# Performance work log

Hardware: AMD Instinct MI355X
Metric: run time of the kernel (lower is better)

Reference implementation:

```python
import jax, jax.numpy as jnp
import numpy as np

B, S, D_IN, D_OUT, BLK = 2, 2048, 4096, 16384, 32
NBLK = D_IN // BLK  # 128


def setup_inputs() -> dict:
    key = jax.random.key(0)
    k_x, k_q, k_s, k_b = jax.random.split(key, 4)
    x = jax.random.normal(k_x, (B, S, D_IN), dtype=jnp.float32)
    # GGML Q8_0: signed 8-bit quants per block of 32
    qs = jax.random.randint(k_q, (D_OUT, NBLK, BLK), -128, 128, dtype=jnp.int32)
    # per-block scales (stand-in for the fp16 'd' field); small magnitude
    scales = jax.random.uniform(k_s, (D_OUT, NBLK), dtype=jnp.float32) * 0.02
    bias = jax.random.normal(k_b, (D_OUT,), dtype=jnp.float32)
    return {"x": x, "qs": qs, "scales": scales, "bias": bias}


def reference(x, qs, scales, bias):
    # _materialize_weight: block dequantize (d * q per block) then cast to input dtype
    # qs: [O, NBLK, BLK], scales: [O, NBLK] -> W: [O, D_IN]
    W = (scales[:, :, None] * qs.astype(x.dtype)).reshape(D_OUT, D_IN)
    # host Linear: y = x @ W^T + b
    y = jnp.einsum('bsd,od->bso', x, W) + bias
    return y
```

## Files before the change

kernel.cpp:

```cpp
#include <hip/hip_runtime.h>
#include <cstdint>
#include <cstddef>

#define M_DIM 4096
#define N_DIM 16384
#define K_DIM 4096
#define NBLK_Q 128

#define BM 256
#define BN 256
#define BK 32
#define KSTEPS (K_DIM / BK)
#define BUFB 16384
#define NBUF 4

typedef int i32x4 __attribute__((ext_vector_type(4)));
typedef int i32x16 __attribute__((ext_vector_type(16)));

#define SFENCE() __builtin_amdgcn_sched_barrier(0)
#define BAR() __builtin_amdgcn_s_barrier()
#define WAITVM(n) asm volatile("s_waitcnt vmcnt(" #n ")")
#define WAITLG0() asm volatile("s_waitcnt lgkmcnt(0)")

__global__ __launch_bounds__(256) void quant_x(const float* __restrict__ x,
                                               char* __restrict__ A8S,
                                               float* __restrict__ sxr) {
  const int m = blockIdx.x;
  const int t = threadIdx.x;
  const float* xr = x + (size_t)m * K_DIM + t * 16;
  float4 v[4];
#pragma unroll
  for (int i = 0; i < 4; ++i) v[i] = ((const float4*)xr)[i];
  float amax = 0.f;
#pragma unroll
  for (int i = 0; i < 4; ++i)
    amax = fmaxf(amax, fmaxf(fmaxf(fabsf(v[i].x), fabsf(v[i].y)),
                             fmaxf(fabsf(v[i].z), fabsf(v[i].w))));
#pragma unroll
  for (int off = 32; off; off >>= 1) amax = fmaxf(amax, __shfl_xor(amax, off, 64));
  __shared__ float wmax[4];
  if ((t & 63) == 0) wmax[t >> 6] = amax;
  __syncthreads();
  amax = fmaxf(fmaxf(wmax[0], wmax[1]), fmaxf(wmax[2], wmax[3]));
  const float inv = 127.0f / amax;
  if (t == 0) sxr[m] = amax / 127.0f;
  unsigned d[4];
#pragma unroll
  for (int i = 0; i < 4; ++i) {
    int q0 = (int)rintf(v[i].x * inv), q1 = (int)rintf(v[i].y * inv);
    int q2 = (int)rintf(v[i].z * inv), q3 = (int)rintf(v[i].w * inv);
    d[i] = (q0 & 0xff) | ((q1 & 0xff) << 8) | ((q2 & 0xff) << 16) | ((q3 & 0xff) << 24);
  }
  const int k32 = t >> 1, kg = t & 1;
  const int mtile = m >> 8, mm = m & 255, m32 = mm >> 5, r = mm & 31;
  int4* dst = (int4*)(A8S + ((size_t)(mtile * 128 + k32)) * 8192 + m32 * 1024 + kg * 512 + r * 16);
  *dst = make_int4(d[0], d[1], d[2], d[3]);
}

__global__ __launch_bounds__(256) void pack_w8(const int* __restrict__ qs,
                                               const float* __restrict__ scales,
                                               char* __restrict__ B8S,
                                               float* __restrict__ swc) {
  const int o = blockIdx.x * 4 + (threadIdx.x >> 6);
  const int l = threadIdx.x & 63;
  const float s0 = scales[(size_t)o * NBLK_Q + l];
  const float s1 = scales[(size_t)o * NBLK_Q + 64 + l];
  float S = fmaxf(s0, s1);
#pragma unroll
  for (int off = 32; off; off >>= 1) S = fmaxf(S, __shfl_xor(S, off, 64));
  if (l == 0) swc[o] = S;
  const float rS = 1.0f / S;
  const int nt = o >> 8, col = o & 255, n32 = col >> 5, c = col & 31;
#pragma unroll
  for (int h = 0; h < 2; ++h) {
    const int nb = l + 64 * h;
    const float ratio = ((h == 0) ? s0 : s1) * rS;
    const int4* q = (const int4*)(qs + ((size_t)o * NBLK_Q + nb) * 32);
    unsigned d[8];
#pragma unroll
    for (int g = 0; g < 8; ++g) {
      int4 v = q[g];
      int a0 = (int)rintf((float)v.x * ratio);
      int a1 = (int)rintf((float)v.y * ratio);
      int a2 = (int)rintf((float)v.z * ratio);
      int a3 = (int)rintf((float)v.w * ratio);
      d[g] = (a0 & 0xff) | ((a1 & 0xff) << 8) | ((a2 & 0xff) << 16) | ((a3 & 0xff) << 24);
    }
    char* dst = B8S + ((size_t)(nt * 128 + nb)) * 8192 + n32 * 1024 + c * 16;
    ((int4*)dst)[0] = make_int4(d[0], d[1], d[2], d[3]);
    ((int4*)(dst + 512))[0] = make_int4(d[4], d[5], d[6], d[7]);
  }
}

__global__ __launch_bounds__(512, 2) void gemm_i8(
    const char* __restrict__ A8S, const char* __restrict__ B8S,
    const float* __restrict__ sxr, const float* __restrict__ swc,
    const float* __restrict__ bias, float* __restrict__ C) {
  __shared__ __align__(16) char lds[NBUF * BUFB];

  const int tid = threadIdx.x;
  const int w = tid >> 6;
  const int l = tid & 63;
  const int wm = w >> 2;
  const int wn = w & 3;

  const int bid = blockIdx.x;
  const int xcd = bid & 7;
  const int k = bid >> 3;
  const int mtile = xcd * 2 + (k & 1);
  const int ntile = k >> 1;
  const int brow = mtile * BM;
  const int bcol = ntile * BN;

  const char* srcA = A8S + (size_t)mtile * 128 * 8192 + w * 1024 + l * 16;
  const char* srcB = B8S + (size_t)ntile * 128 * 8192 + w * 1024 + l * 16;
  const int doffA = w * 1024 + l * 16;
  const int doffB = 8192 + w * 1024 + l * 16;
  const int roffA = wm * 4096 + l * 16;
  const int roffB = 8192 + wn * 2048 + l * 16;

  i32x16 acc[4][2] = {};
  i32x4 a0[4], b0[2], a1[4], b1[2];
  int4 gA0, gB0, gA1, gB1;

  {
    int4 ta0 = *(const int4*)(srcA);
    int4 tb0 = *(const int4*)(srcB);
    int4 ta1 = *(const int4*)(srcA + 8192);
    int4 tb1 = *(const int4*)(srcB + 8192);
    *(int4*)(lds + doffA) = ta0;
    *(int4*)(lds + doffB) = tb0;
    *(int4*)(lds + BUFB + doffA) = ta1;
    *(int4*)(lds + BUFB + doffB) = tb1;
    gA0 = *(const int4*)(srcA + 2 * 8192);
    gB0 = *(const int4*)(srcB + 2 * 8192);
    WAITLG0();
    SFENCE(); BAR(); SFENCE();
#pragma unroll
    for (int i = 0; i < 4; ++i)
      a0[i] = *(const i32x4*)(lds + roffA + i * 1024);
#pragma unroll
    for (int j = 0; j < 2; ++j)
      b0[j] = *(const i32x4*)(lds + roffB + j * 1024);
  }

#define STEP(KT, CA, CB, NA, NB, WA, WB, LA, LB)                               \
  do {                                                                         \
    const char* rb = lds + (((KT) + 1) & 3) * BUFB;                            \
    NA[0] = *(const i32x4*)(rb + roffA);                                       \
    NA[1] = *(const i32x4*)(rb + roffA + 1024);                                \
    NA[2] = *(const i32x4*)(rb + roffA + 2048);                                \
    NA[3] = *(const i32x4*)(rb + roffA + 3072);                                \
    NB[0] = *(const i32x4*)(rb + roffB);                                       \
    NB[1] = *(const i32x4*)(rb + roffB + 1024);                                \
    {                                                                          \
      const int ql = ((KT) + 3 > KSTEPS - 1) ? (KSTEPS - 1) : ((KT) + 3);      \
      LA = *(const int4*)(srcA + (size_t)ql * 8192);                           \
      LB = *(const int4*)(srcB + (size_t)ql * 8192);                           \
    }                                                                          \
    SFENCE();                                                                  \
    __builtin_amdgcn_s_setprio(1);                                             \
    acc[0][0] = __builtin_amdgcn_mfma_i32_32x32x32_i8(CA[0], CB[0], acc[0][0], 0, 0, 0); \
    acc[0][1] = __builtin_amdgcn_mfma_i32_32x32x32_i8(CA[0], CB[1], acc[0][1], 0, 0, 0); \
    acc[1][0] = __builtin_amdgcn_mfma_i32_32x32x32_i8(CA[1], CB[0], acc[1][0], 0, 0, 0); \
    acc[1][1] = __builtin_amdgcn_mfma_i32_32x32x32_i8(CA[1], CB[1], acc[1][1], 0, 0, 0); \
    acc[2][0] = __builtin_amdgcn_mfma_i32_32x32x32_i8(CA[2], CB[0], acc[2][0], 0, 0, 0); \
    acc[2][1] = __builtin_amdgcn_mfma_i32_32x32x32_i8(CA[2], CB[1], acc[2][1], 0, 0, 0); \
    acc[3][0] = __builtin_amdgcn_mfma_i32_32x32x32_i8(CA[3], CB[0], acc[3][0], 0, 0, 0); \
    acc[3][1] = __builtin_amdgcn_mfma_i32_32x32x32_i8(CA[3], CB[1], acc[3][1], 0, 0, 0); \
    __builtin_amdgcn_s_setprio(0);                                             \
    SFENCE();                                                                  \
    WAITVM(2);                                                                 \
    {                                                                          \
      char* wb = lds + (((KT) + 2) & 3) * BUFB;                                \
      *(int4*)(wb + doffA) = WA;                                               \
      *(int4*)(wb + doffB) = WB;                                               \
    }                                                                          \
    SFENCE();                                                                  \
    WAITLG0();                                                                 \
    SFENCE(); BAR(); SFENCE();                                                 \
  } while (0)

  for (int kt = 0; kt < KSTEPS; kt += 2) {
    STEP(kt, a0, b0, a1, b1, gA0, gB0, gA1, gB1);
    STEP(kt + 1, a1, b1, a0, b0, gA1, gB1, gA0, gB0);
  }
#undef STEP

#pragma unroll
  for (int i = 0; i < 4; ++i) {
    const int rb = brow + wm * 128 + i * 32 + 4 * (l >> 5);
#pragma unroll
    for (int j = 0; j < 2; ++j) {
      const int col = bcol + wn * 64 + j * 32 + (l & 31);
      const float Sw = swc[col];
      const float bv = bias[col];
#pragma unroll
      for (int r = 0; r < 16; ++r) {
        const int row = rb + (r & 3) + 8 * (r >> 2);
        C[(size_t)row * N_DIM + col] = (float)acc[i][j][r] * (sxr[row] * Sw) + bv;
      }
    }
  }
}

__global__ void naive_gemm(const float* __restrict__ x, const int* __restrict__ qs,
                           const float* __restrict__ scales, const float* __restrict__ bias,
                           float* __restrict__ y) {
  size_t idx = (size_t)blockIdx.x * 256 + threadIdx.x;
  if (idx >= (size_t)M_DIM * N_DIM) return;
  int o = (int)(idx % N_DIM);
  size_t m = idx / N_DIM;
  const float* xr = x + m * K_DIM;
  const int* q = qs + (size_t)o * K_DIM;
  const float* sc = scales + (size_t)o * NBLK_Q;
  float sum = 0.f;
  for (int nb = 0; nb < NBLK_Q; ++nb) {
    float s = sc[nb];
    float bs = 0.f;
#pragma unroll 8
    for (int b = 0; b < 32; ++b) bs += xr[nb * 32 + b] * (float)q[nb * 32 + b];
    sum += s * bs;
  }
  y[idx] = sum + bias[o];
}

extern "C" void kernel_launch(void* const* d_in, const int* in_sizes, int n_in,
                              void* d_out, int out_size, void* d_ws, size_t ws_size,
                              hipStream_t stream) {
  const float* x = (const float*)d_in[0];
  const int* qs = (const int*)d_in[1];
  const float* scales = (const float*)d_in[2];
  const float* bias = (const float*)d_in[3];
  float* y = (float*)d_out;

  const size_t A8_bytes = (size_t)M_DIM * K_DIM;
  const size_t B8_bytes = (size_t)N_DIM * K_DIM;
  const size_t SX_bytes = (size_t)M_DIM * 4;
  const size_t SW_bytes = (size_t)N_DIM * 4;

  if (ws_size < A8_bytes + B8_bytes + SX_bytes + SW_bytes) {
    size_t total = (size_t)M_DIM * N_DIM;
    naive_gemm<<<(unsigned)((total + 255) / 256), 256, 0, stream>>>(x, qs, scales, bias, y);
    return;
  }

  char* A8S = (char*)d_ws;
  char* B8S = A8S + A8_bytes;
  float* sxr = (float*)(B8S + B8_bytes);
  float* swc = (float*)((char*)sxr + SX_bytes);

  quant_x<<<M_DIM, 256, 0, stream>>>(x, A8S, sxr);
  pack_w8<<<N_DIM / 4, 256, 0, stream>>>(qs, scales, B8S, swc);
  gemm_i8<<<(M_DIM / BM) * (N_DIM / BN), 512, 0, stream>>>(A8S, B8S, sxr, swc, bias, y);
}
```

Baseline: 425.0 us.

## Load B fragments directly from global into registers, bypassing LDS

The B operand is no longer staged through shared memory. Each wave loads its B fragments straight from global memory into registers one step ahead, and only A keeps the 4-buffer LDS pipeline, so the per-stage buffer size is halved. This removes the LDS writes and reads for B and shrinks the LDS footprint. In exchange, the 2 waves that share a wn column fetch the same B fragments separately, which raises global traffic, and the shorter prefetch distance for B may expose memory latency.

```diff
diff --git a/kernel.cpp b/kernel.cpp
--- a/kernel.cpp
+++ b/kernel.cpp
@@ -11,7 +11,7 @@
 #define BN 256
 #define BK 32
 #define KSTEPS (K_DIM / BK)
-#define BUFB 16384
+#define BUFB 8192
 #define NBUF 4
 
 typedef int i32x4 __attribute__((ext_vector_type(4)));
@@ -113,83 +113,81 @@
   const int bcol = ntile * BN;
 
   const char* srcA = A8S + (size_t)mtile * 128 * 8192 + w * 1024 + l * 16;
-  const char* srcB = B8S + (size_t)ntile * 128 * 8192 + w * 1024 + l * 16;
+  const char* srcBf = B8S + (size_t)ntile * 128 * 8192 + wn * 2048 + l * 16;
   const int doffA = w * 1024 + l * 16;
-  const int doffB = 8192 + w * 1024 + l * 16;
   const int roffA = wm * 4096 + l * 16;
-  const int roffB = 8192 + wn * 2048 + l * 16;
 
   i32x16 acc[4][2] = {};
-  i32x4 a0[4], b0[2], a1[4], b1[2];
-  int4 gA0, gB0, gA1, gB1;
+  i32x4 ca0, ca1, ca2, ca3, na0, na1, na2, na3;
+  i32x4 cb0, cb1, nb0, nb1;
+  int4 gaC, gaN;
 
   {
-    int4 ta0 = *(const int4*)(srcA);
-    int4 tb0 = *(const int4*)(srcB);
-    int4 ta1 = *(const int4*)(srcA + 8192);
-    int4 tb1 = *(const int4*)(srcB + 8192);
-    *(int4*)(lds + doffA) = ta0;
-    *(int4*)(lds + doffB) = tb0;
-    *(int4*)(lds + BUFB + doffA) = ta1;
-    *(int4*)(lds + BUFB + doffB) = tb1;
-    gA0 = *(const int4*)(srcA + 2 * 8192);
-    gB0 = *(const int4*)(srcB + 2 * 8192);
+    int4 t0 = *(const int4*)(srcA);
+    int4 t1 = *(const int4*)(srcA + 8192);
+    WAITVM(0);
+    *(int4*)(lds + doffA) = t0;
+    *(int4*)(lds + BUFB + doffA) = t1;
     WAITLG0();
     SFENCE(); BAR(); SFENCE();
-#pragma unroll
-    for (int i = 0; i < 4; ++i)
-      a0[i] = *(const i32x4*)(lds + roffA + i * 1024);
-#pragma unroll
-    for (int j = 0; j < 2; ++j)
-      b0[j] = *(const i32x4*)(lds + roffB + j * 1024);
-  }
-
-#define STEP(KT, CA, CB, NA, NB, WA, WB, LA, LB)                               \
+    cb0 = *(const i32x4*)(srcBf);
+    cb1 = *(const i32x4*)(srcBf + 1024);
+    gaC = *(const int4*)(srcA + 2 * 8192);
+    ca0 = *(const i32x4*)(lds + roffA);
+    ca1 = *(const i32x4*)(lds + roffA + 1024);
+    ca2 = *(const i32x4*)(lds + roffA + 2048);
+    ca3 = *(const i32x4*)(lds + roffA + 3072);
+    WAITVM(1);
+    WAITLG0();
+    SFENCE();
+  }
+
+#define STEP(KT, CA0, CA1, CA2, CA3, NA0, NA1, NA2, NA3, CB0, CB1, NB0, NB1, GAC, GAN) \
   do {                                                                         \
+    WAITVM(1);                  \
     const char* rb = lds + (((KT) + 1) & 3) * BUFB;                            \
-    NA[0] = *(const i32x4*)(rb + roffA);                                       \
-    NA[1] = *(const i32x4*)(rb + roffA + 1024);                                \
-    NA[2] = *(const i32x4*)(rb + roffA + 2048);                                \
-    NA[3] = *(const i32x4*)(rb + roffA + 3072);                                \
-    NB[0] = *(const i32x4*)(rb + roffB);                                       \
-    NB[1] = *(const i32x4*)(rb + roffB + 1024);                                \
+    NA0 = *(const i32x4*)(rb + roffA);                                         \
+    NA1 = *(const i32x4*)(rb + roffA + 1024);                                  \
+    NA2 = *(const i32x4*)(rb + roffA + 2048);                                  \
+    NA3 = *(const i32x4*)(rb + roffA + 3072);                                  \
     {                                                                          \
-      const int ql = ((KT) + 3 > KSTEPS - 1) ? (KSTEPS - 1) : ((KT) + 3);      \
-      LA = *(const int4*)(srcA + (size_t)ql * 8192);                           \
-      LB = *(const int4*)(srcB + (size_t)ql * 8192);                           \
+      const int qf = ((KT) + 1 > KSTEPS - 1) ? (KSTEPS - 1) : ((KT) + 1);      \
+      NB0 = *(const i32x4*)(srcBf + (size_t)qf * 8192);                        \
+      NB1 = *(const i32x4*)(srcBf + (size_t)qf * 8192 + 1024);                 \
+      const int qa = ((KT) + 3 > KSTEPS - 1) ? (KSTEPS - 1) : ((KT) + 3);      \
+      GAN = *(const int4*)(srcA + (size_t)qa * 8192);                          \
     }                                                                          \
     SFENCE();                                                                  \
     __builtin_amdgcn_s_setprio(1);                                             \
-    acc[0][0] = __builtin_amdgcn_mfma_i32_32x32x32_i8(CA[0], CB[0], acc[0][0], 0, 0, 0); \
-    acc[0][1] = __builtin_amdgcn_mfma_i32_32x32x32_i8(CA[0], CB[1], acc[0][1], 0, 0, 0); \
-    acc[1][0] = __builtin_amdgcn_mfma_i32_32x32x32_i8(CA[1], CB[0], acc[1][0], 0, 0, 0); \
-    acc[1][1] = __builtin_amdgcn_mfma_i32_32x32x32_i8(CA[1], CB[1], acc[1][1], 0, 0, 0); \
-    acc[2][0] = __builtin_amdgcn_mfma_i32_32x32x32_i8(CA[2], CB[0], acc[2][0], 0, 0, 0); \
-    acc[2][1] = __builtin_amdgcn_mfma_i32_32x32x32_i8(CA[2], CB[1], acc[2][1], 0, 0, 0); \
-    acc[3][0] = __builtin_amdgcn_mfma_i32_32x32x32_i8(CA[3], CB[0], acc[3][0], 0, 0, 0); \
-    acc[3][1] = __builtin_amdgcn_mfma_i32_32x32x32_i8(CA[3], CB[1], acc[3][1], 0, 0, 0); \
+    acc[0][0] = __builtin_amdgcn_mfma_i32_32x32x32_i8(CA0, CB0, acc[0][0], 0, 0, 0); \
+    acc[0][1] = __builtin_amdgcn_mfma_i32_32x32x32_i8(CA0, CB1, acc[0][1], 0, 0, 0); \
+    acc[1][0] = __builtin_amdgcn_mfma_i32_32x32x32_i8(CA1, CB0, acc[1][0], 0, 0, 0); \
+    acc[1][1] = __builtin_amdgcn_mfma_i32_32x32x32_i8(CA1, CB1, acc[1][1], 0, 0, 0); \
+    acc[2][0] = __builtin_amdgcn_mfma_i32_32x32x32_i8(CA2, CB0, acc[2][0], 0, 0, 0); \
+    acc[2][1] = __builtin_amdgcn_mfma_i32_32x32x32_i8(CA2, CB1, acc[2][1], 0, 0, 0); \
+    acc[3][0] = __builtin_amdgcn_mfma_i32_32x32x32_i8(CA3, CB0, acc[3][0], 0, 0, 0); \
+    acc[3][1] = __builtin_amdgcn_mfma_i32_32x32x32_i8(CA3, CB1, acc[3][1], 0, 0, 0); \
     __builtin_amdgcn_s_setprio(0);                                             \
     SFENCE();                                                                  \
-    WAITVM(2);                                                                 \
+    WAITVM(3);               \
     {                                                                          \
       char* wb = lds + (((KT) + 2) & 3) * BUFB;                                \
-      *(int4*)(wb + doffA) = WA;                                               \
-      *(int4*)(wb + doffB) = WB;                                               \
+      *(int4*)(wb + doffA) = GAC;                                              \
     }                                                                          \
     SFENCE();                                                                  \
-    WAITLG0();                                                                 \
+    WAITLG0();                       \
     SFENCE(); BAR(); SFENCE();                                                 \
   } while (0)
 
   for (int kt = 0; kt < KSTEPS; kt += 2) {
-    STEP(kt, a0, b0, a1, b1, gA0, gB0, gA1, gB1);
-    STEP(kt + 1, a1, b1, a0, b0, gA1, gB1, gA0, gB0);
+    STEP(kt, ca0, ca1, ca2, ca3, na0, na1, na2, na3, cb0, cb1, nb0, nb1, gaC, gaN);
+    STEP(kt + 1, na0, na1, na2, na3, ca0, ca1, ca2, ca3, nb0, nb1, cb0, cb1, gaN, gaC);
   }
 #undef STEP
 
 #pragma unroll
   for (int i = 0; i < 4; ++i) {
-    const int rb = brow + wm * 128 + i * 32 + 4 * (l >> 5);
+    const int rbx = brow + wm * 128 + i * 32 + 4 * (l >> 5);
 #pragma unroll
     for (int j = 0; j < 2; ++j) {
       const int col = bcol + wn * 64 + j * 32 + (l & 31);
@@ -197,7 +195,7 @@
       const float bv = bias[col];
 #pragma unroll
       for (int r = 0; r < 16; ++r) {
-        const int row = rb + (r & 3) + 8 * (r >> 2);
+        const int row = rbx + (r & 3) + 8 * (r >> 2);
         C[(size_t)row * N_DIM + col] = (float)acc[i][j][r] * (sxr[row] * Sw) + bv;
       }
     }
```

Result: slower. 469.7 us (+10.5%).
